# Optimization experiments

Hardware: AMD Instinct MI355X
Metric: run time of the kernel (lower is better)

Reference implementation:

```python
import jax, jax.numpy as jnp
import numpy as np

B, N, D = 8, 2048, 256

def setup_inputs() -> dict:
    key = jax.random.key(0)
    k1, k2, k3, k4 = jax.random.split(key, 4)
    x1 = jax.random.normal(k1, (B, N, D), dtype=jnp.float32)
    x2 = jax.random.normal(k2, (B, N, D), dtype=jnp.float32)
    W = jax.random.normal(k3, (D, D), dtype=jnp.float32) * (1.0 / np.sqrt(D))
    b = jax.random.normal(k4, (D,), dtype=jnp.float32) * 0.01
    return {"x1": x1, "x2": x2, "W": W, "b": b}

def reference(x1, x2, W, b):
    # torch Linear: q = x1 @ W^T + b
    q = jnp.einsum('bnd,ed->bne', x1, W) + b            # [B, N1, D]
    scores = jnp.einsum('bnd,bmd->bnm', q, x2)          # [B, N1, N2]
    scores = jax.nn.softmax(scores, axis=-1)
    x1_updated = jnp.einsum('bnm,bmd->bnd', scores, x2)  # [B, N1, D]
    x2_updated = jnp.einsum('bnm,bnd->bmd', scores, x1)  # scores^T @ x1 -> [B, N2, D]
    return (x1_updated, x2_updated)
```

## Files before the change

### kernel.cpp

```cpp
#include <hip/hip_runtime.h>

#define BB 8
#define NN 2048
#define DD 256

typedef unsigned short u16;
typedef float f32x4 __attribute__((ext_vector_type(4)));
typedef short s16x8 __attribute__((ext_vector_type(8)));
typedef __bf16 bf16x8 __attribute__((ext_vector_type(8)));
typedef _Float16 f16x8 __attribute__((ext_vector_type(8)));
typedef unsigned short u16x4 __attribute__((ext_vector_type(4)));

#define MFMA_BF(a, b, c)                                                       \
  __builtin_amdgcn_mfma_f32_16x16x32_bf16(__builtin_bit_cast(bf16x8, (a)),     \
                                          __builtin_bit_cast(bf16x8, (b)),     \
                                          (c), 0, 0, 0)
#define MFMA_F16(a, b, c)                                                      \
  __builtin_amdgcn_mfma_f32_16x16x32_f16(__builtin_bit_cast(f16x8, (a)),       \
                                         __builtin_bit_cast(f16x8, (b)),       \
                                         (c), 0, 0, 0)

__device__ inline u16 f2bf(float f) {
  union { float f; unsigned u; } v; v.f = f;
  unsigned r = v.u + 0x7FFFu + ((v.u >> 16) & 1u);
  return (u16)(r >> 16);
}
__device__ inline float bf2f(u16 h) {
  union { unsigned u; float f; } v; v.u = ((unsigned)h) << 16;
  return v.f;
}
__device__ inline u16 f2h(float f) {
  _Float16 h = (_Float16)f;
  return __builtin_bit_cast(unsigned short, h);
}
__device__ inline float h2f(u16 h) {
  _Float16 x = __builtin_bit_cast(_Float16, h);
  return (float)x;
}
struct HL { short h, l; };
__device__ inline HL splitbf(float f) {
  HL r;
  u16 hh = f2bf(f);
  r.h = (short)hh;
  r.l = (short)f2bf(f - bf2f(hh));
  return r;
}
__device__ inline void split8(const f32x4 a, const f32x4 c, s16x8& h, s16x8& lo) {
#pragma unroll
  for (int i = 0; i < 4; ++i) {
    HL r = splitbf(a[i]);
    h[i] = r.h; lo[i] = r.l;
  }
#pragma unroll
  for (int i = 0; i < 4; ++i) {
    HL r = splitbf(c[i]);
    h[4 + i] = r.h; lo[4 + i] = r.l;
  }
}
__device__ inline s16x8 cvt8h(const f32x4 a, const f32x4 c) {
  s16x8 h;
#pragma unroll
  for (int i = 0; i < 4; ++i) h[i] = (short)f2h(a[i]);
#pragma unroll
  for (int i = 0; i < 4; ++i) h[4 + i] = (short)f2h(c[i]);
  return h;
}

__device__ inline void gll16(const void* g, void* l) {
  __builtin_amdgcn_global_load_lds(
      (const __attribute__((address_space(1))) unsigned int*)g,
      (__attribute__((address_space(3))) unsigned int*)l, 16, 0, 0);
}

__global__ __launch_bounds__(256) void k_conv2(const float* __restrict__ x1,
                                               const float* __restrict__ x2,
                                               u16* __restrict__ xb1T,
                                               u16* __restrict__ xb2T,
                                               u16* __restrict__ xb2n) {
  __shared__ u16 t[64][68];
  const int zz = blockIdx.z;
  const float* src = (zz < 8) ? x1 : x2;
  u16* dstT = (zz < 8) ? xb1T : xb2T;
  u16* dstN = (zz < 8) ? (u16*)0 : xb2n;
  const int b = zz & 7;
  const int n0 = blockIdx.x * 64;
  const int d0 = blockIdx.y * 64;
  const int tid = threadIdx.x;
  const int r = tid >> 4;
  const int c4 = tid & 15;
#pragma unroll
  for (int rr = 0; rr < 4; ++rr) {
    const int row = r + rr * 16;
    const float4 v = *(const float4*)&src[(size_t)(b * NN + n0 + row) * DD + d0 + c4 * 4];
    u16x4 o2 = {f2h(v.x), f2h(v.y), f2h(v.z), f2h(v.w)};
    if (dstN)
      *(u16x4*)&dstN[(size_t)(b * NN + n0 + row) * DD + d0 + c4 * 4] = o2;
    *(u16x4*)&t[row][c4 * 4] = o2;
  }
  __syncthreads();
  const int d = tid >> 2;
  const int ch = tid & 3;
  u16 buf[16];
#pragma unroll
  for (int j = 0; j < 16; ++j) buf[j] = t[ch * 16 + j][d];
  u16* outp = &dstT[(size_t)(b * DD + d0 + d) * NN + n0 + ch * 16];
  s16x8 v0, v1;
#pragma unroll
  for (int j = 0; j < 8; ++j) { v0[j] = (short)buf[j]; v1[j] = (short)buf[8 + j]; }
  *(s16x8*)outp = v0;
  *(s16x8*)(outp + 8) = v1;
}

__global__ __launch_bounds__(256) void k_qgemm(const float* __restrict__ x1,
                                               const float* __restrict__ W,
                                               const float* __restrict__ bias,
                                               u16* __restrict__ qf) {
  __shared__ char wl[131072];
  const int tid = threadIdx.x;
  const int w = tid >> 6, l = tid & 63, lr = l & 15, lg = l >> 4;
  const int row0 = blockIdx.x * 64 + w * 16;

  s16x8 afh[8], afl[8];
#pragma unroll
  for (int ks = 0; ks < 8; ++ks) {
    const f32x4 a = *(const f32x4*)&x1[(size_t)(row0 + lr) * DD + ks * 32 + lg * 8];
    const f32x4 c = *(const f32x4*)&x1[(size_t)(row0 + lr) * DD + ks * 32 + lg * 8 + 4];
    split8(a, c, afh[ks], afl[ks]);
  }

  const f32x4 zero4 = {0.f, 0.f, 0.f, 0.f};
  f32x4 acc[16];
#pragma unroll
  for (int i = 0; i < 16; ++i) acc[i] = zero4;

  const int er = tid >> 1;
  const int kh = tid & 1;

  for (int eh = 0; eh < 2; ++eh) {
    __syncthreads();
    {
      const int e = eh * 128 + er;
#pragma unroll
      for (int j = 0; j < 16; ++j) {
        const f32x4 a = *(const f32x4*)&W[(size_t)e * DD + kh * 128 + j * 8];
        const f32x4 c = *(const f32x4*)&W[(size_t)e * DD + kh * 128 + j * 8 + 4];
        s16x8 h, lo;
        split8(a, c, h, lo);
        int off = er * 512 + kh * 256 + j * 16;
        off ^= (er & 7) << 4;
        *(s16x8*)(wl + off) = h;
        *(s16x8*)(wl + 65536 + off) = lo;
      }
    }
    __syncthreads();
#pragma unroll
    for (int ct = 0; ct < 8; ++ct) {
      const int el = ct * 16 + lr;
#pragma unroll
      for (int ks = 0; ks < 8; ++ks) {
        int off = el * 512 + ks * 64 + lg * 16;
        off ^= (el & 7) << 4;
        const s16x8 bh = *(const s16x8*)(wl + off);
        const s16x8 bl = *(const s16x8*)(wl + 65536 + off);
        f32x4 acv = acc[eh * 8 + ct];
        acv = MFMA_BF(afh[ks], bh, acv);
        acv = MFMA_BF(afl[ks], bh, acv);
        acv = MFMA_BF(afh[ks], bl, acv);
        acc[eh * 8 + ct] = acv;
      }
    }
  }

#pragma unroll
  for (int i = 0; i < 16; ++i) {
    const int col = (i >> 3) * 128 + (i & 7) * 16 + lr;
    const float bb = bias[col];
#pragma unroll
    for (int r = 0; r < 4; ++r) {
      const int orow = row0 + lg * 4 + r;
      qf[(size_t)orow * DD + col] = f2h(acc[i][r] + bb);
    }
  }
}

__global__ __launch_bounds__(256, 2) void k_flashB(const u16* __restrict__ qf_g,
                                                   const u16* __restrict__ xb2n,
                                                   const u16* __restrict__ xb2T,
                                                   u16* __restrict__ opart,
                                                   float2* __restrict__ ml) {
  __shared__ char smem[69632];
  const int tid = threadIdx.x;
  const int w = tid >> 6, l = tid & 63, lr = l & 15, lg = l >> 4;
  const int bid = blockIdx.x;
  const int b = bid & 7, nt = (bid >> 3) & 31, g = bid >> 8;
  const int n0 = nt * 64;

  s16x8 qfr[8];
  {
    const size_t qoff = (size_t)(b * NN + n0 + w * 16 + lr) * DD;
#pragma unroll
    for (int ks = 0; ks < 8; ++ks)
      qfr[ks] = *(const s16x8*)(qf_g + qoff + ks * 32 + lg * 8);
  }

  const f32x4 zero4 = {0.f, 0.f, 0.f, 0.f};
  f32x4 o[16];
#pragma unroll
  for (int i = 0; i < 16; ++i) o[i] = zero4;
  float M[4] = {-INFINITY, -INFINITY, -INFINITY, -INFINITY};
  float L[4] = {0.f, 0.f, 0.f, 0.f};

  const u16* xnb = xb2n + (size_t)b * NN * DD;
  const u16* xtb = xb2T + (size_t)b * DD * NN;
  char* plds = smem + 65536 + w * 1024;

  const u16* srcN[4];
  const u16* srcT[4];
#pragma unroll
  for (int j = 0; j < 4; ++j) {
    const int idx = j * 4096 + w * 1024 + l * 16;
    const int rowN = idx >> 9;
    const int colN = ((idx & 511) ^ ((rowN & 7) << 4)) >> 1;
    srcN[j] = xnb + (size_t)rowN * DD + colN;
    const int da = (idx >> 6) ^ ((idx >> 8) & 1);
    const int sA = idx ^ ((da & 7) << 4);
    srcT[j] = xtb + (size_t)(sA >> 6) * NN + ((sA & 63) >> 1);
  }

  auto ISSUE = [&](int buf, int m0) {
    char* bN = smem + buf * 32768;
    char* bT = bN + 16384;
#pragma unroll
    for (int j = 0; j < 4; ++j)
      gll16(srcN[j] + (size_t)m0 * DD, bN + j * 4096 + w * 1024);
#pragma unroll
    for (int j = 0; j < 4; ++j)
      gll16(srcT[j] + m0, bT + j * 4096 + w * 1024);
  };

  ISSUE(0, g * 1024);
  __syncthreads();

  for (int t = 0; t < 32; ++t) {
    const int cur = t & 1;
    if (t < 31) ISSUE(cur ^ 1, g * 1024 + (t + 1) * 32);
    const char* bN = smem + cur * 32768;
    const char* bT = bN + 16384;

    __builtin_amdgcn_s_setprio(1);
    f32x4 s0 = zero4, s1 = zero4;
#pragma unroll
    for (int ks = 0; ks < 8; ++ks) {
      int off0 = (lr * 512 + ks * 64 + lg * 16) ^ ((lr & 7) << 4);
      const s16x8 b0 = *(const s16x8*)(bN + off0);
      s0 = MFMA_F16(qfr[ks], b0, s0);
      const int m1 = 16 + lr;
      int off1 = (m1 * 512 + ks * 64 + lg * 16) ^ ((m1 & 7) << 4);
      const s16x8 b1 = *(const s16x8*)(bN + off1);
      s1 = MFMA_F16(qfr[ks], b1, s1);
    }
    __builtin_amdgcn_s_setprio(0);

    float p0[4], p1[4];
#pragma unroll
    for (int r = 0; r < 4; ++r) {
      float tm = fmaxf(s0[r], s1[r]);
      tm = fmaxf(tm, __shfl_xor(tm, 1));
      tm = fmaxf(tm, __shfl_xor(tm, 2));
      tm = fmaxf(tm, __shfl_xor(tm, 4));
      tm = fmaxf(tm, __shfl_xor(tm, 8));
      const float Mn = fmaxf(M[r], tm);
      const float corr = __expf(M[r] - Mn);
      M[r] = Mn;
      p0[r] = __expf(s0[r] - Mn);
      p1[r] = __expf(s1[r] - Mn);
      L[r] = L[r] * corr + p0[r] + p1[r];
#pragma unroll
      for (int dt = 0; dt < 16; ++dt) o[dt][r] *= corr;
    }

#pragma unroll
    for (int r = 0; r < 4; ++r) {
      const int row = lg * 4 + r;
      const int key = (row & 7) << 4;
      int o0 = (row * 64 + lr * 2) ^ key;
      int o1 = (row * 64 + 32 + lr * 2) ^ key;
      *(u16*)(plds + o0) = f2h(p0[r]);
      *(u16*)(plds + o1) = f2h(p1[r]);
    }
    int ra = (lr * 64 + lg * 16) ^ ((lr & 7) << 4);
    const s16x8 pa = *(const s16x8*)(plds + ra);

    __builtin_amdgcn_s_setprio(1);
#pragma unroll
    for (int dt = 0; dt < 16; ++dt) {
      const int dl = dt * 16 + lr;
      int off = (dl * 64 + lg * 16) ^ ((dl & 7) << 4);
      const s16x8 bv = *(const s16x8*)(bT + off);
      o[dt] = MFMA_F16(pa, bv, o[dt]);
    }
    __builtin_amdgcn_s_setprio(0);

    __syncthreads();
  }

#pragma unroll
  for (int r = 0; r < 4; ++r) {
    float s = L[r];
    s += __shfl_xor(s, 1); s += __shfl_xor(s, 2);
    s += __shfl_xor(s, 4); s += __shfl_xor(s, 8);
    L[r] = s;
  }

  const int blin = b * 32 + nt;
  u16* pb = opart + (((size_t)(g * 1024 + blin * 4 + w)) << 12);
#pragma unroll
  for (int dt = 0; dt < 16; ++dt) {
    u16x4 v = {f2h(o[dt][0]), f2h(o[dt][1]), f2h(o[dt][2]), f2h(o[dt][3])};
    *(u16x4*)(pb + ((dt * 64 + l) << 2)) = v;
  }
  if (lr == 0) {
#pragma unroll
    for (int r = 0; r < 4; ++r) {
      float2 v = {M[r], L[r]};
      ml[g * 16384 + b * 2048 + n0 + w * 16 + lg * 4 + r] = v;
    }
  }
}

__global__ __launch_bounds__(256) void k_mergeB(const u16* __restrict__ opart,
                                                const float2* __restrict__ ml,
                                                float* __restrict__ out0,
                                                float* __restrict__ lse) {
  __shared__ float4 cf[16];
  const int bid = blockIdx.x;
  const int blin = bid >> 2, wg = bid & 3;
  const int b = blin >> 5, nt = blin & 31;
  const int tid = threadIdx.x;
  const int row0 = b * 2048 + nt * 64 + wg * 16;
  if (tid < 16) {
    const float2 m0 = ml[row0 + tid];
    const float2 m1 = ml[16384 + row0 + tid];
    const float Mf = fmaxf(m0.x, m1.x);
    const float c0 = __expf(m0.x - Mf);
    const float c1 = __expf(m1.x - Mf);
    const float Lf = m0.y * c0 + m1.y * c1;
    float4 v = {c0, c1, 1.f / Lf, 0.f};
    cf[tid] = v;
    lse[row0 + tid] = Mf + __logf(Lf);
  }
  __syncthreads();
  const int lane = tid & 63;
  const size_t base0 = ((size_t)(blin * 4 + wg)) << 12;
  const size_t base1 = base0 + (1024ull << 12);
#pragma unroll
  for (int k = 0; k < 4; ++k) {
    const int dt = (tid >> 6) * 4 + k;
    const u16x4 v0 = *(const u16x4*)(opart + base0 + ((dt * 64 + lane) << 2));
    const u16x4 v1 = *(const u16x4*)(opart + base1 + ((dt * 64 + lane) << 2));
#pragma unroll
    for (int r = 0; r < 4; ++r) {
      const int i = (lane >> 4) * 4 + r;
      const float4 c = cf[i];
      const float val = (h2f((u16)v0[r]) * c.x + h2f((u16)v1[r]) * c.y) * c.z;
      out0[(size_t)(row0 + i) * DD + dt * 16 + (lane & 15)] = val;
    }
  }
}

__global__ __launch_bounds__(256, 2) void k_passC(const float* __restrict__ x2f,
                                                  const u16* __restrict__ qf_g,
                                                  const u16* __restrict__ xb1T,
                                                  const float* __restrict__ lse,
                                                  u16* __restrict__ opart) {
  __shared__ char smem[69632];
  const int tid = threadIdx.x;
  const int w = tid >> 6, l = tid & 63, lr = l & 15, lg = l >> 4;
  const int bid = blockIdx.x;
  const int b = bid & 7, mt = (bid >> 3) & 31, g = bid >> 8;
  const int m0 = mt * 64;

  s16x8 xf[8];
  {
    const float* xp = x2f + (size_t)(b * NN + m0 + w * 16 + lr) * DD;
#pragma unroll
    for (int ks = 0; ks < 8; ++ks) {
      const f32x4 a = *(const f32x4*)(xp + ks * 32 + lg * 8);
      const f32x4 c = *(const f32x4*)(xp + ks * 32 + lg * 8 + 4);
      xf[ks] = cvt8h(a, c);
    }
  }

  const f32x4 zero4 = {0.f, 0.f, 0.f, 0.f};
  f32x4 o[16];
#pragma unroll
  for (int i = 0; i < 16; ++i) o[i] = zero4;

  const u16* qfb = qf_g + (size_t)b * NN * DD;
  const u16* xtb = xb1T + (size_t)b * DD * NN;
  const float* lsb = lse + (size_t)b * NN;
  char* plds = smem + 65536 + w * 1024;

  const u16* srcQ[4];
  const u16* srcT[4];
#pragma unroll
  for (int j = 0; j < 4; ++j) {
    const int idx = j * 4096 + w * 1024 + l * 16;
    const int rowN = idx >> 9;
    const int colN = ((idx & 511) ^ ((rowN & 7) << 4)) >> 1;
    srcQ[j] = qfb + (size_t)rowN * DD + colN;
    const int da = (idx >> 6) ^ ((idx >> 8) & 1);
    const int sA = idx ^ ((da & 7) << 4);
    srcT[j] = xtb + (size_t)(sA >> 6) * NN + ((sA & 63) >> 1);
  }

  auto ISSUE = [&](int buf, int nn0) {
    char* bQ = smem + buf * 32768;
    char* bT = bQ + 16384;
#pragma unroll
    for (int j = 0; j < 4; ++j)
      gll16(srcQ[j] + (size_t)nn0 * DD, bQ + j * 4096 + w * 1024);
#pragma unroll
    for (int j = 0; j < 4; ++j)
      gll16(srcT[j] + nn0, bT + j * 4096 + w * 1024);
  };

  ISSUE(0, g * 1024);
  __syncthreads();

  for (int t = 0; t < 32; ++t) {
    const int cur = t & 1;
    if (t < 31) ISSUE(cur ^ 1, g * 1024 + (t + 1) * 32);
    const char* bQ = smem + cur * 32768;
    const char* bT = bQ + 16384;

    __builtin_amdgcn_s_setprio(1);
    f32x4 s0 = zero4, s1 = zero4;
#pragma unroll
    for (int ks = 0; ks < 8; ++ks) {
      int off0 = (lr * 512 + ks * 64 + lg * 16) ^ ((lr & 7) << 4);
      const s16x8 b0 = *(const s16x8*)(bQ + off0);
      s0 = MFMA_F16(xf[ks], b0, s0);
      const int n1 = 16 + lr;
      int off1 = (n1 * 512 + ks * 64 + lg * 16) ^ ((n1 & 7) << 4);
      const s16x8 b1 = *(const s16x8*)(bQ + off1);
      s1 = MFMA_F16(xf[ks], b1, s1);
    }
    __builtin_amdgcn_s_setprio(0);

    const int nb = g * 1024 + t * 32;
    const float lv0 = lsb[nb + lr];
    const float lv1 = lsb[nb + 16 + lr];
    float p0[4], p1[4];
#pragma unroll
    for (int r = 0; r < 4; ++r) {
      p0[r] = __expf(s0[r] - lv0);
      p1[r] = __expf(s1[r] - lv1);
    }

#pragma unroll
    for (int r = 0; r < 4; ++r) {
      const int row = lg * 4 + r;
      const int key = (row & 7) << 4;
      int o0 = (row * 64 + lr * 2) ^ key;
      int o1 = (row * 64 + 32 + lr * 2) ^ key;
      *(u16*)(plds + o0) = f2h(p0[r]);
      *(u16*)(plds + o1) = f2h(p1[r]);
    }
    int ra = (lr * 64 + lg * 16) ^ ((lr & 7) << 4);
    const s16x8 pa = *(const s16x8*)(plds + ra);

    __builtin_amdgcn_s_setprio(1);
#pragma unroll
    for (int dt = 0; dt < 16; ++dt) {
      const int dl = dt * 16 + lr;
      int off = (dl * 64 + lg * 16) ^ ((dl & 7) << 4);
      const s16x8 bv = *(const s16x8*)(bT + off);
      o[dt] = MFMA_F16(pa, bv, o[dt]);
    }
    __builtin_amdgcn_s_setprio(0);

    __syncthreads();
  }

  const int blin = b * 32 + mt;
  u16* pb = opart + (((size_t)(g * 1024 + blin * 4 + w)) << 12);
#pragma unroll
  for (int dt = 0; dt < 16; ++dt) {
    u16x4 v = {f2h(o[dt][0]), f2h(o[dt][1]), f2h(o[dt][2]), f2h(o[dt][3])};
    *(u16x4*)(pb + ((dt * 64 + l) << 2)) = v;
  }
}

__global__ __launch_bounds__(256) void k_mergeC(const u16* __restrict__ opart,
                                                float* __restrict__ out1) {
  const int bid = blockIdx.x;
  const int blin = bid >> 2, wg = bid & 3;
  const int b = blin >> 5, mt = blin & 31;
  const int tid = threadIdx.x;
  const int row0 = b * 2048 + mt * 64 + wg * 16;
  const int lane = tid & 63;
  const size_t base0 = ((size_t)(blin * 4 + wg)) << 12;
  const size_t base1 = base0 + (1024ull << 12);
#pragma unroll
  for (int k = 0; k < 4; ++k) {
    const int dt = (tid >> 6) * 4 + k;
    const u16x4 v0 = *(const u16x4*)(opart + base0 + ((dt * 64 + lane) << 2));
    const u16x4 v1 = *(const u16x4*)(opart + base1 + ((dt * 64 + lane) << 2));
#pragma unroll
    for (int r = 0; r < 4; ++r) {
      const int i = (lane >> 4) * 4 + r;
      out1[(size_t)(row0 + i) * DD + dt * 16 + (lane & 15)] =
          h2f((u16)v0[r]) + h2f((u16)v1[r]);
    }
  }
}

extern "C" void kernel_launch(void* const* d_in, const int* in_sizes, int n_in,
                              void* d_out, int out_size, void* d_ws, size_t ws_size,
                              hipStream_t stream) {
  (void)in_sizes; (void)n_in; (void)out_size; (void)ws_size;
  const float* x1 = (const float*)d_in[0];
  const float* x2 = (const float*)d_in[1];
  const float* W  = (const float*)d_in[2];
  const float* bs = (const float*)d_in[3];
  float* out0 = (float*)d_out;
  float* out1 = out0 + (size_t)BB * NN * DD;

  char* ws = (char*)d_ws;
  u16* xb2T  = (u16*)(ws);
  u16* xb1T  = (u16*)(ws + 8388608);
  u16* opart = (u16*)(ws + 16777216);
  u16* xb2n   = (u16*)out0;
  u16* qf     = (u16*)out1;
  float2* ml  = (float2*)((char*)out1 + 8388608);
  float* lseb = (float*)((char*)out1 + 8650752);

  k_conv2<<<dim3(32, 4, 16), 256, 0, stream>>>(x1, x2, xb1T, xb2T, xb2n);
  k_qgemm<<<256, 256, 0, stream>>>(x1, W, bs, qf);
  k_flashB<<<512, 256, 0, stream>>>(qf, xb2n, xb2T, opart, ml);
  k_mergeB<<<1024, 256, 0, stream>>>(opart, ml, out0, lseb);
  k_passC<<<512, 256, 0, stream>>>(x2, qf, xb1T, lseb, opart);
  k_mergeC<<<1024, 256, 0, stream>>>(opart, out1);
}
```

Before: 181.6 us.

## Single-buffer the QK operand tile to cut LDS footprint in attention kernels

The N/Q operand tile used for the score MFMAs is now single-buffered. It is reloaded right after an extra mid-iteration barrier, while the transposed V-side tile stays double-buffered. This shrinks shared memory per block from 68 KB to 52 KB, which could allow more resident blocks per CU. The cost is an extra __syncthreads per iteration, and the next QK tile's load now overlaps only the softmax and PV phase rather than a full iteration.

Result: slower. 187.4 us (+3.2%).

```diff
diff --git a/kernel.cpp b/kernel.cpp
--- a/kernel.cpp
+++ b/kernel.cpp
@@ -188,7 +188,7 @@
                                                    const u16* __restrict__ xb2T,
                                                    u16* __restrict__ opart,
                                                    float2* __restrict__ ml) {
-  __shared__ char smem[69632];
+  __shared__ char smem[53248];
   const int tid = threadIdx.x;
   const int w = tid >> 6, l = tid & 63, lr = l & 15, lg = l >> 4;
   const int bid = blockIdx.x;
@@ -212,7 +212,8 @@
 
   const u16* xnb = xb2n + (size_t)b * NN * DD;
   const u16* xtb = xb2T + (size_t)b * DD * NN;
-  char* plds = smem + 65536 + w * 1024;
+  char* bN = smem;
+  char* plds = smem + 49152 + w * 1024;
 
   const u16* srcN[4];
   const u16* srcT[4];
@@ -227,25 +228,25 @@
     srcT[j] = xtb + (size_t)(sA >> 6) * NN + ((sA & 63) >> 1);
   }
 
-  auto ISSUE = [&](int buf, int m0) {
-    char* bN = smem + buf * 32768;
-    char* bT = bN + 16384;
+  auto ISSUE_N = [&](int m0) {
 #pragma unroll
     for (int j = 0; j < 4; ++j)
       gll16(srcN[j] + (size_t)m0 * DD, bN + j * 4096 + w * 1024);
+  };
+  auto ISSUE_T = [&](int buf, int m0) {
+    char* bT = smem + 16384 + buf * 16384;
 #pragma unroll
     for (int j = 0; j < 4; ++j)
       gll16(srcT[j] + m0, bT + j * 4096 + w * 1024);
   };
 
-  ISSUE(0, g * 1024);
+  ISSUE_N(g * 1024);
+  ISSUE_T(0, g * 1024);
   __syncthreads();
 
   for (int t = 0; t < 32; ++t) {
     const int cur = t & 1;
-    if (t < 31) ISSUE(cur ^ 1, g * 1024 + (t + 1) * 32);
-    const char* bN = smem + cur * 32768;
-    const char* bT = bN + 16384;
+    if (t < 31) ISSUE_T(cur ^ 1, g * 1024 + (t + 1) * 32);
 
     __builtin_amdgcn_s_setprio(1);
     f32x4 s0 = zero4, s1 = zero4;
@@ -260,6 +261,9 @@
       s1 = MFMA_F16(qfr[ks], b1, s1);
     }
     __builtin_amdgcn_s_setprio(0);
+
+    __syncthreads();
+    if (t < 31) ISSUE_N(g * 1024 + (t + 1) * 32);
 
     float p0[4], p1[4];
 #pragma unroll
@@ -291,6 +295,7 @@
     int ra = (lr * 64 + lg * 16) ^ ((lr & 7) << 4);
     const s16x8 pa = *(const s16x8*)(plds + ra);
 
+    const char* bT = smem + 16384 + cur * 16384;
     __builtin_amdgcn_s_setprio(1);
 #pragma unroll
     for (int dt = 0; dt < 16; ++dt) {
@@ -373,7 +378,7 @@
                                                   const u16* __restrict__ xb1T,
                                                   const float* __restrict__ lse,
                                                   u16* __restrict__ opart) {
-  __shared__ char smem[69632];
+  __shared__ char smem[53248];
   const int tid = threadIdx.x;
   const int w = tid >> 6, l = tid & 63, lr = l & 15, lg = l >> 4;
   const int bid = blockIdx.x;
@@ -399,7 +404,8 @@
   const u16* qfb = qf_g + (size_t)b * NN * DD;
   const u16* xtb = xb1T + (size_t)b * DD * NN;
   const float* lsb = lse + (size_t)b * NN;
-  char* plds = smem + 65536 + w * 1024;
+  char* bQ = smem;
+  char* plds = smem + 49152 + w * 1024;
 
   const u16* srcQ[4];
   const u16* srcT[4];
@@ -414,25 +420,25 @@
     srcT[j] = xtb + (size_t)(sA >> 6) * NN + ((sA & 63) >> 1);
   }
 
-  auto ISSUE = [&](int buf, int nn0) {
-    char* bQ = smem + buf * 32768;
-    char* bT = bQ + 16384;
+  auto ISSUE_Q = [&](int nn0) {
 #pragma unroll
     for (int j = 0; j < 4; ++j)
       gll16(srcQ[j] + (size_t)nn0 * DD, bQ + j * 4096 + w * 1024);
+  };
+  auto ISSUE_T = [&](int buf, int nn0) {
+    char* bT = smem + 16384 + buf * 16384;
 #pragma unroll
     for (int j = 0; j < 4; ++j)
       gll16(srcT[j] + nn0, bT + j * 4096 + w * 1024);
   };
 
-  ISSUE(0, g * 1024);
+  ISSUE_Q(g * 1024);
+  ISSUE_T(0, g * 1024);
   __syncthreads();
 
   for (int t = 0; t < 32; ++t) {
     const int cur = t & 1;
-    if (t < 31) ISSUE(cur ^ 1, g * 1024 + (t + 1) * 32);
-    const char* bQ = smem + cur * 32768;
-    const char* bT = bQ + 16384;
+    if (t < 31) ISSUE_T(cur ^ 1, g * 1024 + (t + 1) * 32);
 
     __builtin_amdgcn_s_setprio(1);
     f32x4 s0 = zero4, s1 = zero4;
@@ -448,6 +454,9 @@
     }
     __builtin_amdgcn_s_setprio(0);
 
+    __syncthreads();
+    if (t < 31) ISSUE_Q(g * 1024 + (t + 1) * 32);
+
     const int nb = g * 1024 + t * 32;
     const float lv0 = lsb[nb + lr];
     const float lv1 = lsb[nb + 16 + lr];
@@ -470,6 +479,7 @@
     int ra = (lr * 64 + lg * 16) ^ ((lr & 7) << 4);
     const s16x8 pa = *(const s16x8*)(plds + ra);
 
+    const char* bT = smem + 16384 + cur * 16384;
     __builtin_amdgcn_s_setprio(1);
 #pragma unroll
     for (int dt = 0; dt < 16; ++dt) {
```
